# Optimization experiments

Hardware: AMD Instinct MI355X
Metric: run time of the kernel (lower is better)

## Reference

```python
import jax, jax.numpy as jnp
import numpy as np

NEG = jnp.float32(-1e9)


def setup_inputs() -> dict:
    key = jax.random.key(0)
    ks = jax.random.split(key, 8)
    B, S, D = 8, 2048, 1024
    scale = 1.0 / np.sqrt(D)
    return {
        "xQ": jax.random.normal(ks[0], (B, S, D), jnp.float32),
        "xK": jax.random.normal(ks[1], (B, S, D), jnp.float32),
        "xV": jax.random.normal(ks[2], (B, S, D), jnp.float32),
        "padding_mask": jax.random.randint(ks[3], (B, S), 0, 2, jnp.int32),
        "casual_mask": jnp.ones((B, S), jnp.int32),
        "W_q": jax.random.normal(ks[4], (D, D), jnp.float32) * scale,
        "b_q": jnp.zeros((D,), jnp.float32),
        "W_k": jax.random.normal(ks[5], (D, D), jnp.float32) * scale,
        "b_k": jnp.zeros((D,), jnp.float32),
        "W_v": jax.random.normal(ks[6], (D, D), jnp.float32) * scale,
        "b_v": jnp.zeros((D,), jnp.float32),
    }


def reference(xQ, xK, xV, padding_mask, casual_mask, W_q, b_q, W_k, b_k, W_v, b_v):
    # Linear projections (torch nn.Linear: x @ W.T + b)
    Q = jnp.einsum('bsd,ed->bse', xQ, W_q) + b_q
    K = jnp.einsum('bsd,ed->bse', xK, W_k) + b_k
    V = jnp.einsum('bsd,ed->bse', xV, W_v) + b_v

    # Raw logits (note: original code applies NO 1/sqrt(dk) scaling)
    QKT = jnp.einsum('bqd,bkd->bqk', Q, K)  # [B, Sq, Sk]

    # Additive padding mask: -1e9 on padded key positions
    pad = jnp.where(padding_mask[:, None, :] == 0, NEG, jnp.float32(0.0))
    # Additive causal mask: -1e9 above the diagonal
    Sq, Sk = QKT.shape[1], QKT.shape[2]
    caus = jnp.where(
        jnp.tril(jnp.ones((Sq, Sk), dtype=bool)), jnp.float32(0.0), NEG
    )[None, :, :]
    QKT = QKT + pad + caus

    S = jax.nn.softmax(QKT, axis=-1)
    return jnp.einsum('bqk,bkd->bqd', S, V)
```

## Files before the change

kernel.cpp:

```cpp
#include <hip/hip_runtime.h>

typedef __attribute__((ext_vector_type(4))) float f4;
typedef __attribute__((ext_vector_type(4))) float f32x4;
typedef _Float16 half8 __attribute__((ext_vector_type(8)));

#define DEVI static __device__ __forceinline__

DEVI void gload_lds16(const void* g, void* l) {
  __builtin_amdgcn_global_load_lds(
      (const __attribute__((address_space(1))) void*)g,
      (__attribute__((address_space(3))) void*)l, 16, 0, 0);
}

DEVI int xcd_swz(int id, int n) {
  int q = n >> 3, r = n & 7;
  int x = id & 7, c = id >> 3;
  return (x < r ? x * (q + 1) : r * (q + 1) + (x - r) * q) + c;
}

#define FENCED_BARRIER()                \
  __builtin_amdgcn_sched_barrier(0);    \
  __builtin_amdgcn_s_barrier();         \
  __builtin_amdgcn_sched_barrier(0);

#define SWZ(kgv, rowv) ((((kgv) ^ ((rowv) >> 1)) & 3) * 8)

__global__ __launch_bounds__(256) void cvt_plain(const float* __restrict__ X,
                                                 _Float16* __restrict__ H,
                                                 int n4) {
  int i = blockIdx.x * 256 + threadIdx.x;
  const int stride = gridDim.x * 256;
  typedef _Float16 half4v __attribute__((ext_vector_type(4)));
  for (; i < n4; i += stride) {
    f4 x = ((const f4*)X)[i];
    half4v h;
#pragma unroll
    for (int j = 0; j < 4; ++j) h[j] = (_Float16)x[j];
    ((half4v*)H)[i] = h;
  }
}

__global__ __launch_bounds__(256) void cvt_split(const float* __restrict__ X,
                                                 _Float16* __restrict__ H,
                                                 _Float16* __restrict__ L,
                                                 int n4) {
  int i = blockIdx.x * 256 + threadIdx.x;
  const int stride = gridDim.x * 256;
  typedef _Float16 half4v __attribute__((ext_vector_type(4)));
  for (; i < n4; i += stride) {
    f4 x = ((const f4*)X)[i];
    half4v h, l;
#pragma unroll
    for (int j = 0; j < 4; ++j) {
      h[j] = (_Float16)x[j];
      l[j] = (_Float16)(x[j] - (float)h[j]);
    }
    ((half4v*)H)[i] = h;
    ((half4v*)L)[i] = l;
  }
}

DEVI void acc_zero44(f32x4 (&acc)[4][4]) {
#pragma unroll
  for (int i = 0; i < 4; ++i)
#pragma unroll
    for (int j = 0; j < 4; ++j) acc[i][j] = (f32x4)0.0f;
}
DEVI void acc_zero42(f32x4 (&acc)[4][2]) {
#pragma unroll
  for (int i = 0; i < 4; ++i)
#pragma unroll
    for (int j = 0; j < 2; ++j) acc[i][j] = (f32x4)0.0f;
}

template <int WSPLIT, int OUTMODE>
__global__ __launch_bounds__(512, 2) void proj_fused(
    const float* __restrict__ X, const _Float16* __restrict__ Wh,
    const _Float16* __restrict__ Wl, const float* __restrict__ bias,
    _Float16* __restrict__ OutHi, _Float16* __restrict__ OutLo,
    _Float16* __restrict__ VtOut) {
  extern __shared__ _Float16 lds[];
  constexpr int ACH = 256 * 32;
  constexpr int BCH = 128 * 32;
  constexpr int CHUNK = ACH + BCH * (1 + WSPLIT);
  const int id = xcd_swz(blockIdx.x, gridDim.x);
  const int m0 = (id >> 3) * 256, n0 = (id & 7) * 128;
  const float* A = X + (size_t)m0 * 1024;
  const _Float16* B0 = Wh + (size_t)n0 * 1024;
  const _Float16* B1 = Wl + (size_t)n0 * 1024;
  const int tid = threadIdx.x;
  const int w = tid >> 6, lane = tid & 63;
  const int wm = w >> 1, wn = w & 1;
  const int r16 = lane & 15, kg = lane >> 4;
  f32x4 acc[4][4];
  acc_zero44(acc);
  f4 ra[4];

  auto ALOAD = [&](int t) {
#pragma unroll
    for (int j = 0; j < 2; ++j) {
      int g = tid + j * 512;
      int row = g >> 2, c = g & 3;
      const float* src = A + (size_t)row * 1024 + t * 32 + c * 8;
      ra[2 * j] = *(const f4*)src;
      ra[2 * j + 1] = *(const f4*)(src + 4);
    }
  };
  auto AWRITE = [&](int buf) {
    _Float16* ab = lds + buf * CHUNK;
#pragma unroll
    for (int j = 0; j < 2; ++j) {
      int g = tid + j * 512;
      int row = g >> 2, c = g & 3;
      half8 h;
#pragma unroll
      for (int e = 0; e < 4; ++e) {
        h[e] = (_Float16)ra[2 * j][e];
        h[e + 4] = (_Float16)ra[2 * j + 1][e];
      }
      *(half8*)(ab + (size_t)row * 32 + SWZ(c, row)) = h;
    }
  };
  auto WLOAD = [&](int t, int buf) {
    _Float16* bb = lds + buf * CHUNK + ACH;
    int row = tid >> 2, c = tid & 3;
    int cs = (c ^ (row >> 1)) & 3;
    gload_lds16(B0 + (size_t)row * 1024 + t * 32 + cs * 8, bb + tid * 8);
    if (WSPLIT)
      gload_lds16(B1 + (size_t)row * 1024 + t * 32 + cs * 8,
                  bb + BCH + tid * 8);
  };
  auto COMPUTE = [&](int buf) {
    const _Float16* la = lds + buf * CHUNK;
    const _Float16* lb = la + ACH;
    half8 a[4], b0f[4], b1f[4];
#pragma unroll
    for (int mi = 0; mi < 4; ++mi) {
      int row = wm * 64 + mi * 16 + r16;
      a[mi] = *(const half8*)(la + row * 32 + SWZ(kg, row));
    }
#pragma unroll
    for (int ni = 0; ni < 4; ++ni) {
      int row = wn * 64 + ni * 16 + r16;
      int off = row * 32 + SWZ(kg, row);
      b0f[ni] = *(const half8*)(lb + off);
      if (WSPLIT) b1f[ni] = *(const half8*)(lb + BCH + off);
    }
    __builtin_amdgcn_s_setprio(1);
#pragma unroll
    for (int mi = 0; mi < 4; ++mi)
#pragma unroll
      for (int ni = 0; ni < 4; ++ni) {
        acc[mi][ni] = __builtin_amdgcn_mfma_f32_16x16x32_f16(
            a[mi], b0f[ni], acc[mi][ni], 0, 0, 0);
        if (WSPLIT)
          acc[mi][ni] = __builtin_amdgcn_mfma_f32_16x16x32_f16(
              a[mi], b1f[ni], acc[mi][ni], 0, 0, 0);
      }
    __builtin_amdgcn_s_setprio(0);
  };

  const int NS = 32;
  WLOAD(0, 0);
  ALOAD(0);
  asm volatile("s_waitcnt vmcnt(0)" ::: "memory");
  __builtin_amdgcn_sched_barrier(0);
  AWRITE(0);
  asm volatile("s_waitcnt lgkmcnt(0)" ::: "memory");
  FENCED_BARRIER();
  for (int t = 0; t < NS; ++t) {
    if (t + 1 < NS) {
      WLOAD(t + 1, (t + 1) & 1);
      ALOAD(t + 1);
    }
    COMPUTE(t & 1);
    if (t + 1 < NS) {
      asm volatile("s_waitcnt vmcnt(0)" ::: "memory");
      __builtin_amdgcn_sched_barrier(0);
      AWRITE((t + 1) & 1);
      asm volatile("s_waitcnt lgkmcnt(0)" ::: "memory");
      FENCED_BARRIER();
    }
  }

  float bcol[4];
#pragma unroll
  for (int ni = 0; ni < 4; ++ni) bcol[ni] = bias[n0 + wn * 64 + ni * 16 + r16];

  if (OUTMODE != 2) {
#pragma unroll
    for (int mi = 0; mi < 4; ++mi) {
      int row = m0 + wm * 64 + mi * 16 + kg * 4;
#pragma unroll
      for (int ni = 0; ni < 4; ++ni) {
        int col = n0 + wn * 64 + ni * 16 + r16;
#pragma unroll
        for (int j = 0; j < 4; ++j) {
          float v = acc[mi][ni][j] + bcol[ni];
          _Float16 h = (_Float16)v;
          OutHi[(size_t)(row + j) * 1024 + col] = h;
          if (OUTMODE == 0)
            OutLo[(size_t)(row + j) * 1024 + col] = (_Float16)(v - (float)h);
        }
      }
    }
  } else {
    __syncthreads();
    _Float16(*T)[256] = (_Float16(*)[256])lds;
#pragma unroll
    for (int mi = 0; mi < 4; ++mi) {
      int ml = wm * 64 + mi * 16 + kg * 4;
#pragma unroll
      for (int ni = 0; ni < 4; ++ni) {
        int nl = wn * 64 + ni * 16 + r16;
#pragma unroll
        for (int j = 0; j < 4; ++j)
          T[nl][ml + j] = (_Float16)(acc[mi][ni][j] + bcol[ni]);
      }
    }
    __syncthreads();
    const int b = m0 >> 11;
    const int s0 = m0 & 2047;
#pragma unroll
    for (int r = 0; r < 8; ++r) {
      int flat = tid + r * 512;
      int n = flat >> 5, c = flat & 31;
      half8 v = *(const half8*)&T[n][c * 8];
      *(half8*)(VtOut + (size_t)b * (1024 * 2048) + (size_t)(n0 + n) * 2048 +
                s0 + c * 8) = v;
    }
  }
}

__global__ __launch_bounds__(512, 4) void qk_eng(
    const _Float16* __restrict__ Qh, const _Float16* __restrict__ Ql,
    const _Float16* __restrict__ Kh, float* __restrict__ Lg, int bbase) {
  extern __shared__ _Float16 lds[];
  constexpr int CHUNK = 12288;
  const int id = xcd_swz(blockIdx.x, gridDim.x);
  const int y = id / 144;
  int t = id % 144;
  int g4 = 0, base = 0;
  while (t >= base + (g4 + 1) * 4) { base += (g4 + 1) * 4; ++g4; }
  const int rem = t - base;
  const int qt = g4 * 4 + rem / (g4 + 1);
  const int kt = rem % (g4 + 1);
  const int b = bbase + y;
  const size_t boff = (size_t)b * (2048 * 1024);
  const _Float16* A0 = Qh + boff + (size_t)(qt * 64) * 1024;
  const _Float16* A1 = Ql + boff + (size_t)(qt * 64) * 1024;
  const _Float16* B0 = Kh + boff + (size_t)(kt * 256) * 1024;
  const int tid = threadIdx.x;
  const int w = tid >> 6, lane = tid & 63;
  const int r16 = lane & 15, kg = lane >> 4;
  const int wn = w;
  f32x4 acc[4][2];
  acc_zero42(acc);

  auto STAGE = [&](int t_, int buf) {
    _Float16* base_ = lds + buf * CHUNK;
    {
      int g = tid & 255;
      int row = g >> 2, c = g & 3;
      int cs = (c ^ (row >> 1)) & 3;
      const _Float16* src = (tid < 256) ? A0 : A1;
      _Float16* dst = base_ + ((tid < 256) ? 0 : 2048);
      gload_lds16(src + (size_t)row * 1024 + t_ * 32 + cs * 8, dst + g * 8);
    }
#pragma unroll
    for (int j = 0; j < 2; ++j) {
      int g = tid + j * 512;
      int row = g >> 2, c = g & 3;
      int cs = (c ^ (row >> 1)) & 3;
      gload_lds16(B0 + (size_t)row * 1024 + t_ * 32 + cs * 8,
                  base_ + 4096 + g * 8);
    }
  };
  auto COMPUTE = [&](int buf) {
    const _Float16* la = lds + buf * CHUNK;
    half8 a0[4], a1[4], bf[2];
#pragma unroll
    for (int mi = 0; mi < 4; ++mi) {
      int row = mi * 16 + r16;
      int off = row * 32 + SWZ(kg, row);
      a0[mi] = *(const half8*)(la + off);
      a1[mi] = *(const half8*)(la + 2048 + off);
    }
#pragma unroll
    for (int ni = 0; ni < 2; ++ni) {
      int row = wn * 32 + ni * 16 + r16;
      bf[ni] = *(const half8*)(la + 4096 + row * 32 + SWZ(kg, row));
    }
    __builtin_amdgcn_s_setprio(1);
#pragma unroll
    for (int mi = 0; mi < 4; ++mi)
#pragma unroll
      for (int ni = 0; ni < 2; ++ni) {
        acc[mi][ni] = __builtin_amdgcn_mfma_f32_16x16x32_f16(
            a0[mi], bf[ni], acc[mi][ni], 0, 0, 0);
        acc[mi][ni] = __builtin_amdgcn_mfma_f32_16x16x32_f16(
            a1[mi], bf[ni], acc[mi][ni], 0, 0, 0);
      }
    __builtin_amdgcn_s_setprio(0);
  };

  const int NS = 32;
  STAGE(0, 0);
  STAGE(1, 1);
  int tt = 0;
  for (; tt < NS - 1; ++tt) {
    asm volatile("s_waitcnt vmcnt(3)" ::: "memory");
    FENCED_BARRIER();
    if (tt + 2 < NS) STAGE(tt + 2, (tt + 2) % 3);
    COMPUTE(tt % 3);
  }
  asm volatile("s_waitcnt vmcnt(0)" ::: "memory");
  FENCED_BARRIER();
  COMPUTE(tt % 3);

  float* L = Lg + (size_t)y * (2048 * 2048);
#pragma unroll
  for (int mi = 0; mi < 4; ++mi) {
    int row = qt * 64 + mi * 16 + kg * 4;
#pragma unroll
    for (int ni = 0; ni < 2; ++ni) {
      int col = kt * 256 + wn * 32 + ni * 16 + r16;
#pragma unroll
      for (int j = 0; j < 4; ++j)
        L[(size_t)(row + j) * 2048 + col] = acc[mi][ni][j];
    }
  }
}

__global__ __launch_bounds__(512, 4) void pv_eng(
    const float* __restrict__ Lg, const _Float16* __restrict__ Vt,
    float* __restrict__ Out, int bbase) {
  extern __shared__ _Float16 lds[];
  constexpr int CHUNK = 8192;
  const int id = xcd_swz(blockIdx.x, gridDim.x);
  const int y = id >> 7;
  const int qt = (id & 127) >> 3, nt = id & 7;
  const int b = bbase + y;
  const _Float16* P = (const _Float16*)(Lg + (size_t)y * (2048 * 2048));
  const _Float16* A0 = P + (size_t)(qt * 128) * 4096;
  const _Float16* B0 =
      Vt + (size_t)b * (1024 * 2048) + (size_t)(nt * 128) * 2048;
  const int NS = (qt + 1) * 4;
  const int tid = threadIdx.x;
  const int w = tid >> 6, lane = tid & 63;
  const int wm = w >> 2, wn = w & 3;
  const int r16 = lane & 15, kg = lane >> 4;
  f32x4 acc[4][2];
  acc_zero42(acc);

  auto STAGE = [&](int t_, int buf) {
    _Float16* base_ = lds + buf * CHUNK;
    {
      int row = tid >> 2, c = tid & 3;
      int cs = (c ^ (row >> 1)) & 3;
      gload_lds16(A0 + (size_t)row * 4096 + t_ * 32 + cs * 8, base_ + tid * 8);
      gload_lds16(B0 + (size_t)row * 2048 + t_ * 32 + cs * 8,
                  base_ + 4096 + tid * 8);
    }
  };
  auto COMPUTE = [&](int buf) {
    const _Float16* la = lds + buf * CHUNK;
    half8 a[4], bf[2];
#pragma unroll
    for (int mi = 0; mi < 4; ++mi) {
      int row = wm * 64 + mi * 16 + r16;
      a[mi] = *(const half8*)(la + row * 32 + SWZ(kg, row));
    }
#pragma unroll
    for (int ni = 0; ni < 2; ++ni) {
      int row = wn * 32 + ni * 16 + r16;
      bf[ni] = *(const half8*)(la + 4096 + row * 32 + SWZ(kg, row));
    }
    __builtin_amdgcn_s_setprio(1);
#pragma unroll
    for (int mi = 0; mi < 4; ++mi)
#pragma unroll
      for (int ni = 0; ni < 2; ++ni)
        acc[mi][ni] = __builtin_amdgcn_mfma_f32_16x16x32_f16(
            a[mi], bf[ni], acc[mi][ni], 0, 0, 0);
    __builtin_amdgcn_s_setprio(0);
  };

  STAGE(0, 0);
  STAGE(1, 1);
  int tt = 0;
  for (; tt < NS - 1; ++tt) {
    asm volatile("s_waitcnt vmcnt(2)" ::: "memory");
    FENCED_BARRIER();
    if (tt + 2 < NS) STAGE(tt + 2, (tt + 2) % 3);
    COMPUTE(tt % 3);
  }
  asm volatile("s_waitcnt vmcnt(0)" ::: "memory");
  FENCED_BARRIER();
  COMPUTE(tt % 3);

#pragma unroll
  for (int mi = 0; mi < 4; ++mi) {
    int row = qt * 128 + wm * 64 + mi * 16 + kg * 4;
#pragma unroll
    for (int ni = 0; ni < 2; ++ni) {
      int col = nt * 128 + wn * 32 + ni * 16 + r16;
#pragma unroll
      for (int j = 0; j < 4; ++j)
        Out[(size_t)(b * 2048 + row + j) * 1024 + col] = acc[mi][ni][j];
    }
  }
}

__global__ __launch_bounds__(256) void softmax_kernel(
    float* __restrict__ Lg, const int* __restrict__ pad, int bbase) {
  const int q = blockIdx.x;
  const int y = blockIdx.y;
  const int b = bbase + y;
  const int tid = threadIdx.x;
  float* row = Lg + (size_t)y * (2048 * 2048) + (size_t)q * 2048;
  _Float16* prow = (_Float16*)row;
  const int* pb = pad + (size_t)b * 2048;
  const int kend = ((q >> 8) + 1) << 8;
  float v[8];
  int nv = 0;
  float mx = -3.0e38f;
  for (int k = tid; k <= q; k += 256) {
    float l = row[k];
    if (pb[k] == 0) l += -1.0e9f;
    v[nv++] = l;
    mx = fmaxf(mx, l);
  }
  __shared__ float red[4];
  for (int o = 32; o; o >>= 1) mx = fmaxf(mx, __shfl_xor(mx, o));
  if ((tid & 63) == 0) red[tid >> 6] = mx;
  __syncthreads();
  mx = fmaxf(fmaxf(red[0], red[1]), fmaxf(red[2], red[3]));
  __syncthreads();
  float s = 0.f;
  for (int i = 0; i < nv; ++i) s += expf(v[i] - mx);
  for (int o = 32; o; o >>= 1) s += __shfl_xor(s, o);
  if ((tid & 63) == 0) red[tid >> 6] = s;
  __syncthreads();
  s = red[0] + red[1] + red[2] + red[3];
  const float inv = 1.0f / s;
  int i = 0;
  for (int k = tid; k <= q; k += 256) {
    prow[k] = (_Float16)(expf(v[i] - mx) * inv);
    ++i;
  }
  for (int k = q + 1 + tid; k < kend; k += 256) prow[k] = (_Float16)0.0f;
}

__global__ __launch_bounds__(512) void fix_f(const int* __restrict__ pad,
                                             int* __restrict__ fb) {
  const int b = threadIdx.x >> 6, k = threadIdx.x & 63;
  unsigned long long m = __ballot(pad[b * 2048 + k] != 0);
  if (k == 0) fb[b] = m ? (__ffsll((long long)m) - 1) : 64;
}

__global__ __launch_bounds__(256) void fix_qrow2(
    const float* __restrict__ xQ, const float* __restrict__ Wq,
    const float* __restrict__ bq, const int* __restrict__ fb,
    float* __restrict__ Qrow) {
  const int b = blockIdx.y;
  const int f = fb[b];
  const int tid = threadIdx.x;
  const int e = blockIdx.x * 16 + (tid >> 4);
  const int l16 = tid & 15;
  __shared__ float xq[1024];
  for (int q = 0; q < f; ++q) {
    *(f4*)&xq[tid * 4] = ((const f4*)(xQ + (size_t)(b * 2048 + q) * 1024))[tid];
    __syncthreads();
    float a = 0.f;
#pragma unroll
    for (int it = 0; it < 16; ++it) {
      int d = l16 * 4 + it * 64;
      f4 ww = *(const f4*)(Wq + (size_t)e * 1024 + d);
      a += xq[d] * ww[0] + xq[d + 1] * ww[1] + xq[d + 2] * ww[2] +
           xq[d + 3] * ww[3];
    }
    for (int o = 8; o; o >>= 1) a += __shfl_xor(a, o);
    if (l16 == 0) Qrow[((size_t)b * 64 + q) * 1024 + e] = a + bq[e];
    __syncthreads();
  }
}

__global__ __launch_bounds__(256) void fix_qb0(const float* __restrict__ bk,
                                               const int* __restrict__ fb,
                                               const float* __restrict__ Qrow,
                                               float* __restrict__ qb0) {
  const int q = blockIdx.x, b = blockIdx.y;
  if (q >= fb[b]) return;
  const int tid = threadIdx.x;
  const float* qr = Qrow + ((size_t)b * 64 + q) * 1024;
  float p = 0.f;
  for (int e = tid; e < 1024; e += 256) p += qr[e] * bk[e];
  __shared__ float red[4];
  for (int o = 32; o; o >>= 1) p += __shfl_xor(p, o);
  if ((tid & 63) == 0) red[tid >> 6] = p;
  __syncthreads();
  if (tid == 0) qb0[b * 64 + q] = red[0] + red[1] + red[2] + red[3];
}

__global__ __launch_bounds__(256) void fix_g2(const float* __restrict__ Wk,
                                              const int* __restrict__ fb,
                                              const float* __restrict__ Qrow,
                                              float* __restrict__ Gpart) {
  const int b = blockIdx.y;
  const int f = fb[b];
  const int tid = threadIdx.x;
  const int ddblk = blockIdx.x & 3, es = blockIdx.x >> 2;
  const int dd = ddblk * 256 + tid;
  __shared__ float qc[128];
  for (int q = 0; q < f; ++q) {
    if (tid < 32)
      *(f4*)&qc[tid * 4] =
          ((const f4*)(Qrow + ((size_t)b * 64 + q) * 1024 + es * 128))[tid];
    __syncthreads();
    float g = 0.f;
    for (int e = 0; e < 128; ++e)
      g += qc[e] * Wk[(size_t)(es * 128 + e) * 1024 + dd];
    Gpart[(((size_t)es * 8 + b) * 64 + q) * 1024 + dd] = g;
    __syncthreads();
  }
}

__global__ __launch_bounds__(256) void fix_logit2(
    const float* __restrict__ xK, const int* __restrict__ pad,
    const int* __restrict__ fb, const float* __restrict__ Gpart,
    const float* __restrict__ qb0, float* __restrict__ lrow) {
  const int b = blockIdx.y;
  const int f = fb[b];
  const int tid = threadIdx.x;
  const int k = blockIdx.x * 16 + (tid >> 4);
  const int l16 = tid & 15;
  __shared__ float Gs[1024];
  for (int q = 0; q < f; ++q) {
    f4 s = (f4)0.0f;
#pragma unroll
    for (int es = 0; es < 8; ++es)
      s += ((const f4*)(Gpart + (((size_t)es * 8 + b) * 64 + q) * 1024))[tid];
    *(f4*)&Gs[tid * 4] = s;
    __syncthreads();
    float a = 0.f;
#pragma unroll
    for (int it = 0; it < 16; ++it) {
      int d = l16 * 4 + it * 64;
      f4 x = *(const f4*)(xK + (size_t)(b * 2048 + k) * 1024 + d);
      a += x[0] * Gs[d] + x[1] * Gs[d + 1] + x[2] * Gs[d + 2] +
           x[3] * Gs[d + 3];
    }
    for (int o = 8; o; o >>= 1) a += __shfl_xor(a, o);
    if (l16 == 0) {
      float l = a + qb0[b * 64 + q];
      if (pad[b * 2048 + k] == 0) l += -1.0e9f;
      if (k > q) l += -1.0e9f;
      lrow[((size_t)b * 64 + q) * 2048 + k] = l;
    }
    __syncthreads();
  }
}

__global__ __launch_bounds__(256) void fix_sm(const int* __restrict__ fb,
                                              float* __restrict__ lrow,
                                              float* __restrict__ srow) {
  const int q = blockIdx.x, b = blockIdx.y;
  if (q >= fb[b]) return;
  const int tid = threadIdx.x;
  float* row = lrow + ((size_t)b * 64 + q) * 2048;
  float v[8];
  float mx = -3.0e38f;
#pragma unroll
  for (int i = 0; i < 8; ++i) {
    v[i] = row[tid + i * 256];
    mx = fmaxf(mx, v[i]);
  }
  __shared__ float red[4];
  for (int o = 32; o; o >>= 1) mx = fmaxf(mx, __shfl_xor(mx, o));
  if ((tid & 63) == 0) red[tid >> 6] = mx;
  __syncthreads();
  mx = fmaxf(fmaxf(red[0], red[1]), fmaxf(red[2], red[3]));
  __syncthreads();
  float s = 0.f;
#pragma unroll
  for (int i = 0; i < 8; ++i) {
    v[i] = expf(v[i] - mx);
    s += v[i];
  }
#pragma unroll
  for (int i = 0; i < 8; ++i) row[tid + i * 256] = v[i];
  for (int o = 32; o; o >>= 1) s += __shfl_xor(s, o);
  if ((tid & 63) == 0) red[tid >> 6] = s;
  __syncthreads();
  if (tid == 0) srow[b * 64 + q] = red[0] + red[1] + red[2] + red[3];
}

__global__ __launch_bounds__(256) void fix_pv2(
    const _Float16* __restrict__ Vt, const int* __restrict__ fb,
    const float* __restrict__ lrow, const float* __restrict__ srow,
    float* __restrict__ Out) {
  const int b = blockIdx.y;
  const int f = fb[b];
  const int tid = threadIdx.x;
  const int d = blockIdx.x * 16 + (tid >> 4);
  const int l16 = tid & 15;
  __shared__ float ps[2048];
  for (int q = 0; q < f; ++q) {
    const f4* src = (const f4*)(lrow + ((size_t)b * 64 + q) * 2048);
    *(f4*)&ps[tid * 8] = src[tid * 2];
    *(f4*)&ps[tid * 8 + 4] = src[tid * 2 + 1];
    __syncthreads();
    float o = 0.f;
#pragma unroll
    for (int it = 0; it < 16; ++it) {
      int k = l16 * 8 + it * 128;
      half8 vv = *(const half8*)(Vt + (size_t)b * (1024 * 2048) +
                                 (size_t)d * 2048 + k);
      o += (float)vv[0] * ps[k] + (float)vv[1] * ps[k + 1] +
           (float)vv[2] * ps[k + 2] + (float)vv[3] * ps[k + 3] +
           (float)vv[4] * ps[k + 4] + (float)vv[5] * ps[k + 5] +
           (float)vv[6] * ps[k + 6] + (float)vv[7] * ps[k + 7];
    }
    for (int of = 8; of; of >>= 1) o += __shfl_xor(o, of);
    if (l16 == 0)
      Out[(size_t)(b * 2048 + q) * 1024 + d] = o * (1.0f / srow[b * 64 + q]);
    __syncthreads();
  }
}

extern "C" void kernel_launch(void* const* d_in, const int* in_sizes, int n_in,
                              void* d_out, int out_size, void* d_ws,
                              size_t ws_size, hipStream_t stream) {
  const float* xQ = (const float*)d_in[0];
  const float* xK = (const float*)d_in[1];
  const float* xV = (const float*)d_in[2];
  const int* pad = (const int*)d_in[3];
  const float* Wq = (const float*)d_in[5];
  const float* bq = (const float*)d_in[6];
  const float* Wk = (const float*)d_in[7];
  const float* bk = (const float*)d_in[8];
  const float* Wv = (const float*)d_in[9];
  const float* bv = (const float*)d_in[10];
  float* Out = (float*)d_out;

  const size_t MB = (size_t)1 << 20;
  char* wsb = (char*)d_ws;
  _Float16* Qh = (_Float16*)(wsb);
  _Float16* Ql = (_Float16*)(wsb + 32 * MB);
  _Float16* Kh = (_Float16*)(wsb + 64 * MB);
  _Float16* Vt = (_Float16*)(wsb + 96 * MB);
  float* Lg = (float*)(wsb + 128 * MB);

  size_t avail = (ws_size > 128 * MB) ? ws_size - 128 * MB : 0;
  int G = (int)(avail / (16 * MB));
  if (G > 8) G = 8;
  if (G < 1) G = 1;

  _Float16* Wqh = (_Float16*)(wsb + 128 * MB);
  _Float16* Wql = (_Float16*)(wsb + 130 * MB);
  _Float16* Wkh = (_Float16*)(wsb + 132 * MB);
  _Float16* Wkl = (_Float16*)(wsb + 134 * MB);
  _Float16* Wvh = (_Float16*)(wsb + 136 * MB);

  const int SM_P = 65536;
  const int SM_V = 65536;
  const int SM_QK = 73728;
  const int SM_PV = 49152;
  (void)hipFuncSetAttribute((const void*)&proj_fused<1, 0>,
                            hipFuncAttributeMaxDynamicSharedMemorySize, SM_P);
  (void)hipFuncSetAttribute((const void*)&proj_fused<1, 1>,
                            hipFuncAttributeMaxDynamicSharedMemorySize, SM_P);
  (void)hipFuncSetAttribute((const void*)&proj_fused<0, 2>,
                            hipFuncAttributeMaxDynamicSharedMemorySize, SM_V);
  (void)hipFuncSetAttribute((const void*)&qk_eng,
                            hipFuncAttributeMaxDynamicSharedMemorySize, SM_QK);
  (void)hipFuncSetAttribute((const void*)&pv_eng,
                            hipFuncAttributeMaxDynamicSharedMemorySize, SM_PV);

  dim3 blk(256), eblk(512);

  cvt_split<<<dim3(1024), blk, 0, stream>>>(Wq, Wqh, Wql, 262144);
  cvt_split<<<dim3(1024), blk, 0, stream>>>(Wk, Wkh, Wkl, 262144);
  cvt_plain<<<dim3(1024), blk, 0, stream>>>(Wv, Wvh, 262144);

  proj_fused<0, 2><<<dim3(512), eblk, SM_V, stream>>>(xV, Wvh, Wvh, bv,
                                                      nullptr, nullptr, Vt);
  proj_fused<1, 1><<<dim3(512), eblk, SM_P, stream>>>(xK, Wkh, Wkl, bk, Kh,
                                                      nullptr, nullptr);
  proj_fused<1, 0><<<dim3(512), eblk, SM_P, stream>>>(xQ, Wqh, Wql, bq, Qh, Ql,
                                                      nullptr);

  for (int bbase = 0; bbase < 8; bbase += G) {
    int nb = (8 - bbase < G) ? (8 - bbase) : G;
    qk_eng<<<dim3(144 * nb), eblk, SM_QK, stream>>>(Qh, Ql, Kh, Lg, bbase);
    softmax_kernel<<<dim3(2048, nb), blk, 0, stream>>>(Lg, pad, bbase);
    pv_eng<<<dim3(128 * nb), eblk, SM_PV, stream>>>(Lg, Vt, Out, bbase);
  }

  int* fb = (int*)(wsb);
  float* qb0 = (float*)(wsb + 4 * 1024);
  float* srow = (float*)(wsb + 8 * 1024);
  float* Qrow = (float*)(wsb + 1 * MB);
  float* Gpart = (float*)(wsb + 4 * MB);
  float* lrow = (float*)(wsb + 20 * MB);

  fix_f<<<dim3(1), dim3(512), 0, stream>>>(pad, fb);
  fix_qrow2<<<dim3(64, 8), blk, 0, stream>>>(xQ, Wq, bq, fb, Qrow);
  fix_qb0<<<dim3(64, 8), blk, 0, stream>>>(bk, fb, Qrow, qb0);
  fix_g2<<<dim3(32, 8), blk, 0, stream>>>(Wk, fb, Qrow, Gpart);
  fix_logit2<<<dim3(128, 8), blk, 0, stream>>>(xK, pad, fb, Gpart, qb0, lrow);
  fix_sm<<<dim3(64, 8), blk, 0, stream>>>(fb, lrow, srow);
  fix_pv2<<<dim3(64, 8), blk, 0, stream>>>(Vt, fb, lrow, srow, Out);
}
```

Before: 547.5 us.

## Pre-convert activations to fp16 and use smaller-tile projection GEMM with direct LDS loads

Adds a proj3 kernel that takes fp16 activations, already converted by a separate cvt_plain pass into workspace. This lets the A tile be streamed with global_load_lds into a 3-stage LDS ring, using 128x128 tiles and higher occupancy (launch bounds of 4 blocks). It replaces the old path, which read fp32 activations inside the GEMM and converted them there. The cost is an extra full read and write pass over each 64 MB input, and the new path only runs when the workspace is at least 165 MB, otherwise falling back to the old kernels.

After: 496.5 us. 1.1x faster.

```diff
diff --git a/kernel.cpp b/kernel.cpp
--- a/kernel.cpp
+++ b/kernel.cpp
@@ -71,6 +71,133 @@
   for (int i = 0; i < 4; ++i)
 #pragma unroll
     for (int j = 0; j < 2; ++j) acc[i][j] = (f32x4)0.0f;
+}
+
+template <int WSPLIT, int OUTMODE>
+__global__ __launch_bounds__(512, 4) void proj3(
+    const _Float16* __restrict__ X, const _Float16* __restrict__ Wh,
+    const _Float16* __restrict__ Wl, const float* __restrict__ bias,
+    _Float16* __restrict__ OutHi, _Float16* __restrict__ OutLo,
+    _Float16* __restrict__ VtOut) {
+  extern __shared__ _Float16 lds[];
+  constexpr int ACH = 128 * 32;
+  constexpr int BCH = 128 * 32;
+  constexpr int CHUNK = ACH + BCH * (1 + WSPLIT);
+  const int id = xcd_swz(blockIdx.x, gridDim.x);
+  const int m0 = (id >> 3) * 128, n0 = (id & 7) * 128;
+  const _Float16* A0 = X + (size_t)m0 * 1024;
+  const _Float16* B0 = Wh + (size_t)n0 * 1024;
+  const _Float16* B1 = Wl + (size_t)n0 * 1024;
+  const int tid = threadIdx.x;
+  const int w = tid >> 6, lane = tid & 63;
+  const int wm = w >> 2, wn = w & 3;
+  const int r16 = lane & 15, kg = lane >> 4;
+  f32x4 acc[4][2];
+  acc_zero42(acc);
+
+  auto STAGE = [&](int t, int buf) {
+    _Float16* base = lds + buf * CHUNK;
+    int row = tid >> 2, c = tid & 3;
+    int cs = (c ^ (row >> 1)) & 3;
+    size_t src = (size_t)row * 1024 + t * 32 + cs * 8;
+    gload_lds16(A0 + src, base + tid * 8);
+    gload_lds16(B0 + src, base + ACH + tid * 8);
+    if (WSPLIT) gload_lds16(B1 + src, base + ACH + BCH + tid * 8);
+  };
+  auto COMPUTE = [&](int buf) {
+    const _Float16* la = lds + buf * CHUNK;
+    const _Float16* lb = la + ACH;
+    half8 a[4], b0f[2], b1f[2];
+#pragma unroll
+    for (int mi = 0; mi < 4; ++mi) {
+      int row = wm * 64 + mi * 16 + r16;
+      a[mi] = *(const half8*)(la + row * 32 + SWZ(kg, row));
+    }
+#pragma unroll
+    for (int ni = 0; ni < 2; ++ni) {
+      int row = wn * 32 + ni * 16 + r16;
+      int off = row * 32 + SWZ(kg, row);
+      b0f[ni] = *(const half8*)(lb + off);
+      if (WSPLIT) b1f[ni] = *(const half8*)(lb + BCH + off);
+    }
+    __builtin_amdgcn_s_setprio(1);
+#pragma unroll
+    for (int mi = 0; mi < 4; ++mi)
+#pragma unroll
+      for (int ni = 0; ni < 2; ++ni) {
+        acc[mi][ni] = __builtin_amdgcn_mfma_f32_16x16x32_f16(
+            a[mi], b0f[ni], acc[mi][ni], 0, 0, 0);
+        if (WSPLIT)
+          acc[mi][ni] = __builtin_amdgcn_mfma_f32_16x16x32_f16(
+              a[mi], b1f[ni], acc[mi][ni], 0, 0, 0);
+      }
+    __builtin_amdgcn_s_setprio(0);
+  };
+
+  const int NS = 32;
+  STAGE(0, 0);
+  STAGE(1, 1);
+  int tt = 0;
+  for (; tt < NS - 1; ++tt) {
+    if constexpr (WSPLIT)
+      asm volatile("s_waitcnt vmcnt(3)" ::: "memory");
+    else
+      asm volatile("s_waitcnt vmcnt(2)" ::: "memory");
+    FENCED_BARRIER();
+    if (tt + 2 < NS) STAGE(tt + 2, (tt + 2) % 3);
+    COMPUTE(tt % 3);
+  }
+  asm volatile("s_waitcnt vmcnt(0)" ::: "memory");
+  FENCED_BARRIER();
+  COMPUTE(tt % 3);
+
+  float bcol[2];
+#pragma unroll
+  for (int ni = 0; ni < 2; ++ni) bcol[ni] = bias[n0 + wn * 32 + ni * 16 + r16];
+
+  if (OUTMODE != 2) {
+#pragma unroll
+    for (int mi = 0; mi < 4; ++mi) {
+      int row = m0 + wm * 64 + mi * 16 + kg * 4;
+#pragma unroll
+      for (int ni = 0; ni < 2; ++ni) {
+        int col = n0 + wn * 32 + ni * 16 + r16;
+#pragma unroll
+        for (int j = 0; j < 4; ++j) {
+          float v = acc[mi][ni][j] + bcol[ni];
+          _Float16 h = (_Float16)v;
+          OutHi[(size_t)(row + j) * 1024 + col] = h;
+          if (OUTMODE == 0)
+            OutLo[(size_t)(row + j) * 1024 + col] = (_Float16)(v - (float)h);
+        }
+      }
+    }
+  } else {
+    __syncthreads();
+    _Float16(*T)[128] = (_Float16(*)[128])lds;
+#pragma unroll
+    for (int mi = 0; mi < 4; ++mi) {
+      int ml = wm * 64 + mi * 16 + kg * 4;
+#pragma unroll
+      for (int ni = 0; ni < 2; ++ni) {
+        int nl = wn * 32 + ni * 16 + r16;
+#pragma unroll
+        for (int j = 0; j < 4; ++j)
+          T[nl][ml + j] = (_Float16)(acc[mi][ni][j] + bcol[ni]);
+      }
+    }
+    __syncthreads();
+    const int b = m0 >> 11;
+    const int s0 = m0 & 2047;
+#pragma unroll
+    for (int r = 0; r < 4; ++r) {
+      int flat = tid + r * 512;
+      int n = flat >> 4, c = flat & 15;
+      half8 v = *(const half8*)&T[n][c * 8];
+      *(half8*)(VtOut + (size_t)b * (1024 * 2048) + (size_t)(n0 + n) * 2048 +
+                s0 + c * 8) = v;
+    }
+  }
 }
 
 template <int WSPLIT, int OUTMODE>
@@ -657,22 +784,23 @@
   if (G > 8) G = 8;
   if (G < 1) G = 1;
 
-  _Float16* Wqh = (_Float16*)(wsb + 128 * MB);
-  _Float16* Wql = (_Float16*)(wsb + 130 * MB);
-  _Float16* Wkh = (_Float16*)(wsb + 132 * MB);
-  _Float16* Wkl = (_Float16*)(wsb + 134 * MB);
-  _Float16* Wvh = (_Float16*)(wsb + 136 * MB);
-
-  const int SM_P = 65536;
-  const int SM_V = 65536;
+  const int SM_P1 = 73728;
+  const int SM_P0 = 49152;
+  const int SM_F = 65536;
   const int SM_QK = 73728;
   const int SM_PV = 49152;
+  (void)hipFuncSetAttribute((const void*)&proj3<1, 0>,
+                            hipFuncAttributeMaxDynamicSharedMemorySize, SM_P1);
+  (void)hipFuncSetAttribute((const void*)&proj3<1, 1>,
+                            hipFuncAttributeMaxDynamicSharedMemorySize, SM_P1);
+  (void)hipFuncSetAttribute((const void*)&proj3<0, 2>,
+                            hipFuncAttributeMaxDynamicSharedMemorySize, SM_P0);
   (void)hipFuncSetAttribute((const void*)&proj_fused<1, 0>,
-                            hipFuncAttributeMaxDynamicSharedMemorySize, SM_P);
+                            hipFuncAttributeMaxDynamicSharedMemorySize, SM_F);
   (void)hipFuncSetAttribute((const void*)&proj_fused<1, 1>,
-                            hipFuncAttributeMaxDynamicSharedMemorySize, SM_P);
+                            hipFuncAttributeMaxDynamicSharedMemorySize, SM_F);
   (void)hipFuncSetAttribute((const void*)&proj_fused<0, 2>,
-                            hipFuncAttributeMaxDynamicSharedMemorySize, SM_V);
+                            hipFuncAttributeMaxDynamicSharedMemorySize, SM_F);
   (void)hipFuncSetAttribute((const void*)&qk_eng,
                             hipFuncAttributeMaxDynamicSharedMemorySize, SM_QK);
   (void)hipFuncSetAttribute((const void*)&pv_eng,
@@ -680,16 +808,49 @@
 
   dim3 blk(256), eblk(512);
 
-  cvt_split<<<dim3(1024), blk, 0, stream>>>(Wq, Wqh, Wql, 262144);
-  cvt_split<<<dim3(1024), blk, 0, stream>>>(Wk, Wkh, Wkl, 262144);
-  cvt_plain<<<dim3(1024), blk, 0, stream>>>(Wv, Wvh, 262144);
-
-  proj_fused<0, 2><<<dim3(512), eblk, SM_V, stream>>>(xV, Wvh, Wvh, bv,
-                                                      nullptr, nullptr, Vt);
-  proj_fused<1, 1><<<dim3(512), eblk, SM_P, stream>>>(xK, Wkh, Wkl, bk, Kh,
-                                                      nullptr, nullptr);
-  proj_fused<1, 0><<<dim3(512), eblk, SM_P, stream>>>(xQ, Wqh, Wql, bq, Qh, Ql,
-                                                      nullptr);
+  if (ws_size >= 165 * MB) {
+    {
+      _Float16* sX = (_Float16*)(wsb);
+      _Float16* sW = (_Float16*)(wsb + 32 * MB);
+      cvt_plain<<<dim3(2048), blk, 0, stream>>>(xV, sX, 4194304);
+      cvt_plain<<<dim3(1024), blk, 0, stream>>>(Wv, sW, 262144);
+      proj3<0, 2><<<dim3(1024), eblk, SM_P0, stream>>>(sX, sW, sW, bv, nullptr,
+                                                       nullptr, Vt);
+    }
+    {
+      _Float16* sX = (_Float16*)(wsb);
+      _Float16* sWh = (_Float16*)(wsb + 32 * MB);
+      _Float16* sWl = (_Float16*)(wsb + 34 * MB);
+      cvt_plain<<<dim3(2048), blk, 0, stream>>>(xK, sX, 4194304);
+      cvt_split<<<dim3(1024), blk, 0, stream>>>(Wk, sWh, sWl, 262144);
+      proj3<1, 1><<<dim3(1024), eblk, SM_P1, stream>>>(sX, sWh, sWl, bk, Kh,
+                                                       nullptr, nullptr);
+    }
+    {
+      _Float16* sX = (_Float16*)(wsb + 128 * MB);
+      _Float16* sWh = (_Float16*)(wsb + 160 * MB);
+      _Float16* sWl = (_Float16*)(wsb + 162 * MB);
+      cvt_plain<<<dim3(2048), blk, 0, stream>>>(xQ, sX, 4194304);
+      cvt_split<<<dim3(1024), blk, 0, stream>>>(Wq, sWh, sWl, 262144);
+      proj3<1, 0><<<dim3(1024), eblk, SM_P1, stream>>>(sX, sWh, sWl, bq, Qh,
+                                                       Ql, nullptr);
+    }
+  } else {
+    _Float16* Wqh = (_Float16*)(wsb + 128 * MB);
+    _Float16* Wql = (_Float16*)(wsb + 130 * MB);
+    _Float16* Wkh = (_Float16*)(wsb + 132 * MB);
+    _Float16* Wkl = (_Float16*)(wsb + 134 * MB);
+    _Float16* Wvh = (_Float16*)(wsb + 136 * MB);
+    cvt_split<<<dim3(1024), blk, 0, stream>>>(Wq, Wqh, Wql, 262144);
+    cvt_split<<<dim3(1024), blk, 0, stream>>>(Wk, Wkh, Wkl, 262144);
+    cvt_plain<<<dim3(1024), blk, 0, stream>>>(Wv, Wvh, 262144);
+    proj_fused<0, 2><<<dim3(512), eblk, SM_F, stream>>>(xV, Wvh, Wvh, bv,
+                                                        nullptr, nullptr, Vt);
+    proj_fused<1, 1><<<dim3(512), eblk, SM_F, stream>>>(xK, Wkh, Wkl, bk, Kh,
+                                                        nullptr, nullptr);
+    proj_fused<1, 0><<<dim3(512), eblk, SM_F, stream>>>(xQ, Wqh, Wql, bq, Qh,
+                                                        Ql, nullptr);
+  }
 
   for (int bbase = 0; bbase < 8; bbase += G) {
     int nb = (8 - bbase < G) ? (8 - bbase) : G;
```
